# Kernel tuning notes

Measured on AMD Instinct MI355X. Metric: run time of the kernel, lower is better.

Reference implementation:

```python
import jax, jax.numpy as jnp
import numpy as np

B, S, D_IN, D_HID, D_OUT = 32, 512, 768, 3072, 768


def setup_inputs() -> dict:
    key = jax.random.key(0)
    k1, k2, k3, k4 = jax.random.split(key, 4)
    init_k = float(np.sqrt(1.0 / D_IN))
    init_k2 = float(np.sqrt(1.0 / D_HID))
    x = jax.random.normal(k1, (B, S, D_IN), dtype=jnp.float32)
    in_weight = jax.random.uniform(k2, (D_HID, D_IN), dtype=jnp.float32, minval=-init_k, maxval=init_k)
    in_bias = jax.random.uniform(k3, (D_HID,), dtype=jnp.float32, minval=-init_k, maxval=init_k)
    out_weight = jax.random.uniform(k4, (D_HID, D_OUT), dtype=jnp.float32, minval=-init_k2, maxval=init_k2)
    return {"x": x, "in_weight": in_weight, "in_bias": in_bias, "out_weight": out_weight}


def reference(x, in_weight, in_bias, out_weight):
    # flatten leading dims to tokens: [B*S, D_IN]
    lead = x.shape[:-1]
    xt = x.reshape(-1, in_weight.shape[1])
    # hidden = GELU(x @ W_in^T + b)   (in_weight stored [hidden, in])
    h = jax.nn.gelu(jnp.einsum('td,hd->th', xt, in_weight) + in_bias, approximate=False)
    # out = hidden @ W_out            (out_weight stored [hidden, out]; no output bias)
    out = jnp.einsum('th,ho->to', h, out_weight)
    return out.reshape(*lead, out_weight.shape[1])
```

## Files before the change

### kernel.cpp

```cpp
#include <hip/hip_runtime.h>

typedef short bf16x8 __attribute__((ext_vector_type(8)));
typedef float f32x4  __attribute__((ext_vector_type(4)));

__device__ __forceinline__ unsigned short f2bf(float f) {
    unsigned int u = __float_as_uint(f);
    u += 0x7FFFu + ((u >> 16) & 1u);
    return (unsigned short)(u >> 16);
}

__device__ __forceinline__ float gelu_f(float x) {
    float x2 = x * x;
    float u = x * (-1.5957691216f - 0.0713548162f * x2);
    float e = __expf(u);
    return x * __builtin_amdgcn_rcpf(1.0f + e);
}

__global__ void cvt_f32_bf16(const float* __restrict__ in,
                             unsigned short* __restrict__ out, int n4) {
    int stride = gridDim.x * blockDim.x;
    for (int i = blockIdx.x * blockDim.x + threadIdx.x; i < n4; i += stride) {
        float4 v = ((const float4*)in)[i];
        ushort4 r;
        r.x = f2bf(v.x); r.y = f2bf(v.y); r.z = f2bf(v.z); r.w = f2bf(v.w);
        ((ushort4*)out)[i] = r;
    }
}

__global__ void transpose_cvt(const float* __restrict__ in,
                              unsigned short* __restrict__ out, int H, int O) {
    __shared__ float tile[32][33];
    int o0 = blockIdx.x * 32, h0 = blockIdx.y * 32;
    int tx = threadIdx.x, ty = threadIdx.y;
    #pragma unroll
    for (int r = 0; r < 32; r += 8)
        tile[ty + r][tx] = in[(size_t)(h0 + ty + r) * O + o0 + tx];
    __syncthreads();
    #pragma unroll
    for (int r = 0; r < 32; r += 8) {
        int o = ty + r;
        out[(size_t)(o0 + o) * H + h0 + tx] = f2bf(tile[tx][o]);
    }
}

template <int EPI, int K, int N, int BN>
__global__ __launch_bounds__(512, 2) void gemm_bt(
    const unsigned short* __restrict__ A,
    const unsigned short* __restrict__ B,
    const float* __restrict__ bias,
    void* __restrict__ Cp) {
    constexpr int NREP = BN / 64;
    constexpr int BHALF = 32768;
    constexpr int LBUF = BHALF + BN * 128;
    __shared__ __align__(16) char lds[2 * LBUF];
    const int t = threadIdx.x;
    const int w = t >> 6, l = t & 63;
    constexpr int ntiles = N / BN;

    int bid = blockIdx.x;
    int nwg = gridDim.x;
    int wgid = ((nwg & 7) == 0) ? ((bid & 7) * (nwg >> 3) + (bid >> 3)) : bid;
    const int mt = wgid / ntiles, nt = wgid % ntiles;
    const int m0 = mt << 8, n0 = nt * BN;
    const int wr = w >> 2, wc = w & 3;

    const int rA = t >> 3;
    const int sl = (t & 7) ^ (rA & 7);

    auto stage = [&](int kt, char* dst) {
        const int kc = kt * 64 + sl * 8;
        #pragma unroll
        for (int i = 0; i < 4; ++i) {
            const unsigned short* ga = A + (size_t)(m0 + i * 64 + rA) * K + kc;
            char* la = dst + i * 8192 + (w << 10);
            __builtin_amdgcn_global_load_lds((const __attribute__((address_space(1))) void*)ga,
                                             (__attribute__((address_space(3))) void*)la, 16, 0, 0);
        }
        #pragma unroll
        for (int i = 0; i < NREP; ++i) {
            const unsigned short* gb = B + (size_t)(n0 + i * 64 + rA) * K + kc;
            char* lb = dst + BHALF + i * 8192 + (w << 10);
            __builtin_amdgcn_global_load_lds((const __attribute__((address_space(1))) void*)gb,
                                             (__attribute__((address_space(3))) void*)lb, 16, 0, 0);
        }
    };

    const int swz = ((l >> 4) ^ (l & 7)) << 4;
    const int aoff0 = (wr * 128 + (l & 15)) * 128 + swz;
    const int aoffX = aoff0 ^ 64;
    const int boff0 = BHALF + (wc * (BN / 4) + (l & 15)) * 128 + swz;
    const int boffX = boff0 ^ 64;

    f32x4 acc[8][NREP];
    {
        f32x4 z = {0.f, 0.f, 0.f, 0.f};
        #pragma unroll
        for (int i = 0; i < 8; ++i)
            #pragma unroll
            for (int j = 0; j < NREP; ++j) acc[i][j] = z;
    }

    constexpr int NT = K >> 6;
    stage(0, lds);
    __builtin_amdgcn_sched_barrier(0);
    asm volatile("" ::: "memory");
    stage(1, lds + LBUF);

    for (int kt = 0; kt < NT; ++kt) {
        if constexpr (NREP == 4)
            asm volatile("s_waitcnt vmcnt(8)\n\ts_barrier" ::: "memory");
        else
            asm volatile("s_waitcnt vmcnt(7)\n\ts_barrier" ::: "memory");
        __builtin_amdgcn_sched_barrier(0);
        const char* base = lds + (kt & 1) * LBUF;
        bf16x8 av[4][2], bv[NREP][2];
        #pragma unroll
        for (int ni = 0; ni < NREP; ++ni) {
            bv[ni][0] = *(const bf16x8*)(base + boff0 + ni * 2048);
            bv[ni][1] = *(const bf16x8*)(base + boffX + ni * 2048);
        }
        #pragma unroll
        for (int mi = 0; mi < 4; ++mi) {
            av[mi][0] = *(const bf16x8*)(base + aoff0 + mi * 2048);
            av[mi][1] = *(const bf16x8*)(base + aoffX + mi * 2048);
        }
        #pragma unroll
        for (int ks = 0; ks < 2; ++ks)
            #pragma unroll
            for (int mi = 0; mi < 4; ++mi)
                #pragma unroll
                for (int ni = 0; ni < NREP; ++ni)
                    acc[mi][ni] = __builtin_amdgcn_mfma_f32_16x16x32_bf16(
                        av[mi][ks], bv[ni][ks], acc[mi][ni], 0, 0, 0);
        #pragma unroll
        for (int mi = 0; mi < 4; ++mi) {
            av[mi][0] = *(const bf16x8*)(base + aoff0 + (4 + mi) * 2048);
            av[mi][1] = *(const bf16x8*)(base + aoffX + (4 + mi) * 2048);
        }
        #pragma unroll
        for (int ks = 0; ks < 2; ++ks)
            #pragma unroll
            for (int mi = 0; mi < 4; ++mi)
                #pragma unroll
                for (int ni = 0; ni < NREP; ++ni)
                    acc[4 + mi][ni] = __builtin_amdgcn_mfma_f32_16x16x32_bf16(
                        av[mi][ks], bv[ni][ks], acc[4 + mi][ni], 0, 0, 0);
        __builtin_amdgcn_sched_barrier(0);
        asm volatile("s_waitcnt lgkmcnt(0)\n\ts_barrier" ::: "memory");
        __builtin_amdgcn_sched_barrier(0);
        if (kt + 2 < NT) stage(kt + 2, lds + (kt & 1) * LBUF);
    }

    if constexpr (EPI == 0) {
        unsigned short* Cb = (unsigned short*)Cp;
        #pragma unroll
        for (int ni = 0; ni < NREP; ++ni) {
            int col = n0 + wc * (BN / 4) + ni * 16 + (l & 15);
            float bvs = bias[col];
            #pragma unroll
            for (int mi = 0; mi < 8; ++mi) {
                int rbase = m0 + wr * 128 + mi * 16 + ((l >> 4) << 2);
                #pragma unroll
                for (int j = 0; j < 4; ++j) {
                    float v = acc[mi][ni][j] + bvs;
                    Cb[(size_t)(rbase + j) * N + col] = f2bf(gelu_f(v));
                }
            }
        }
    } else {
        float* Cf = (float*)Cp;
        #pragma unroll
        for (int ni = 0; ni < NREP; ++ni) {
            int col = n0 + wc * (BN / 4) + ni * 16 + (l & 15);
            #pragma unroll
            for (int mi = 0; mi < 8; ++mi) {
                int rbase = m0 + wr * 128 + mi * 16 + ((l >> 4) << 2);
                #pragma unroll
                for (int j = 0; j < 4; ++j)
                    Cf[(size_t)(rbase + j) * N + col] = acc[mi][ni][j];
            }
        }
    }
}

extern "C" void kernel_launch(void* const* d_in, const int* in_sizes, int n_in,
                              void* d_out, int out_size, void* d_ws, size_t ws_size,
                              hipStream_t stream) {
    const float* x  = (const float*)d_in[0];
    const float* w1 = (const float*)d_in[1];
    const float* b1 = (const float*)d_in[2];
    const float* w2 = (const float*)d_in[3];
    float* out = (float*)d_out;

    const int T = 16384, DIN = 768, DH = 3072, DOUT = 768;

    unsigned short* xb  = (unsigned short*)d_ws;
    unsigned short* w1b = xb  + (size_t)T * DIN;
    unsigned short* w2t = w1b + (size_t)DH * DIN;
    unsigned short* h   = w2t + (size_t)DOUT * DH;

    size_t fixed = ((size_t)T * DIN + (size_t)DH * DIN + (size_t)DOUT * DH) * 2;
    int CH = T;
    while (CH > 256 && fixed + (size_t)CH * DH * 2 > ws_size) CH >>= 1;

    cvt_f32_bf16<<<2048, 256, 0, stream>>>(x, xb, T * DIN / 4);
    cvt_f32_bf16<<<1024, 256, 0, stream>>>(w1, w1b, DH * DIN / 4);
    transpose_cvt<<<dim3(DOUT / 32, DH / 32), dim3(32, 8), 0, stream>>>(w2, w2t, DH, DOUT);

    for (int c0 = 0; c0 < T; c0 += CH) {
        gemm_bt<0, 768, 3072, 256><<<(CH / 256) * (DH / 256), 512, 0, stream>>>(
            xb + (size_t)c0 * DIN, w1b, b1, h);
        gemm_bt<1, 3072, 768, 192><<<(CH / 256) * (DOUT / 192), 512, 0, stream>>>(
            h, w2t, b1, out + (size_t)c0 * DOUT);
    }
}
```

Measured before the change: 193.7 us.

## Shrink GEMM tiles to 256x128x32 with higher occupancy and a new LDS swizzle

Reworks the bf16 GEMM kernel from 256xBN tiles with K-step 64 to 256x128 tiles with K-step 32. LDS per block drops to 48KB and launch bounds rise to 4 blocks per CU, with an 8-wave 4x2 layout where each wave computes 64x64. The staging and fragment addressing use a new XOR swizzle, and the pipeline always issues a stage so the vmcnt count stays fixed. The aim is more occupancy and better latency hiding, at the cost of less data reuse per tile, more barriers per unit of K, and twice as many blocks.

After: 207.6 us. 1.07x slower.

```diff
diff --git a/kernel.cpp b/kernel.cpp
--- a/kernel.cpp
+++ b/kernel.cpp
@@ -43,143 +43,137 @@
     }
 }
 
-template <int EPI, int K, int N, int BN>
-__global__ __launch_bounds__(512, 2) void gemm_bt(
+template <int EPI, int K, int N>
+__global__ __launch_bounds__(512, 4) void gemm_bt(
     const unsigned short* __restrict__ A,
     const unsigned short* __restrict__ B,
     const float* __restrict__ bias,
     void* __restrict__ Cp) {
-    constexpr int NREP = BN / 64;
-    constexpr int BHALF = 32768;
-    constexpr int LBUF = BHALF + BN * 128;
+    constexpr int BHALF = 16384;
+    constexpr int LBUF  = 24576;
     __shared__ __align__(16) char lds[2 * LBUF];
     const int t = threadIdx.x;
     const int w = t >> 6, l = t & 63;
-    constexpr int ntiles = N / BN;
+    constexpr int ntiles = N >> 7;
 
     int bid = blockIdx.x;
     int nwg = gridDim.x;
     int wgid = ((nwg & 7) == 0) ? ((bid & 7) * (nwg >> 3) + (bid >> 3)) : bid;
     const int mt = wgid / ntiles, nt = wgid % ntiles;
-    const int m0 = mt << 8, n0 = nt * BN;
-    const int wr = w >> 2, wc = w & 3;
-
-    const int rA = t >> 3;
-    const int sl = (t & 7) ^ (rA & 7);
+    const int m0 = mt << 8, n0 = nt << 7;
+    const int wr = w >> 1, wc = w & 1;
 
     auto stage = [&](int kt, char* dst) {
-        const int kc = kt * 64 + sl * 8;
-        #pragma unroll
-        for (int i = 0; i < 4; ++i) {
-            const unsigned short* ga = A + (size_t)(m0 + i * 64 + rA) * K + kc;
-            char* la = dst + i * 8192 + (w << 10);
-            __builtin_amdgcn_global_load_lds((const __attribute__((address_space(1))) void*)ga,
-                                             (__attribute__((address_space(3))) void*)la, 16, 0, 0);
+        const int kb = kt << 5;
+        #pragma unroll
+        for (int p = 0; p < 2; ++p) {
+            int idx = p * 512 + t;
+            int prow = idx >> 3;
+            int lg = (idx & 7) ^ (prow & 7);
+            const unsigned short* ga =
+                A + (size_t)(m0 + (lg >> 2) * 128 + prow) * K + kb + (lg & 3) * 8;
+            __builtin_amdgcn_global_load_lds(
+                (const __attribute__((address_space(1))) void*)ga,
+                (__attribute__((address_space(3))) void*)(dst + idx * 16), 16, 0, 0);
         }
-        #pragma unroll
-        for (int i = 0; i < NREP; ++i) {
-            const unsigned short* gb = B + (size_t)(n0 + i * 64 + rA) * K + kc;
-            char* lb = dst + BHALF + i * 8192 + (w << 10);
-            __builtin_amdgcn_global_load_lds((const __attribute__((address_space(1))) void*)gb,
-                                             (__attribute__((address_space(3))) void*)lb, 16, 0, 0);
+        {
+            int prow = t >> 3;
+            int lg = (t & 7) ^ (prow & 7);
+            const unsigned short* gb =
+                B + (size_t)(n0 + (lg >> 2) * 64 + prow) * K + kb + (lg & 3) * 8;
+            __builtin_amdgcn_global_load_lds(
+                (const __attribute__((address_space(1))) void*)gb,
+                (__attribute__((address_space(3))) void*)(dst + BHALF + t * 16), 16, 0, 0);
         }
     };
 
-    const int swz = ((l >> 4) ^ (l & 7)) << 4;
-    const int aoff0 = (wr * 128 + (l & 15)) * 128 + swz;
-    const int aoffX = aoff0 ^ 64;
-    const int boff0 = BHALF + (wc * (BN / 4) + (l & 15)) * 128 + swz;
-    const int boffX = boff0 ^ 64;
-
-    f32x4 acc[8][NREP];
+    const int ks = l >> 4, lr = l & 15;
+    int aoff[4], boff[4];
+    #pragma unroll
+    for (int mi = 0; mi < 4; ++mi) {
+        int prow = (wr & 1) * 64 + mi * 16 + lr;
+        int lg   = ((wr >> 1) << 2) + ks;
+        aoff[mi] = prow * 128 + ((lg ^ (prow & 7)) << 4);
+    }
+    #pragma unroll
+    for (int ni = 0; ni < 4; ++ni) {
+        int prow = ni * 16 + lr;
+        int lg   = (wc << 2) + ks;
+        boff[ni] = BHALF + prow * 128 + ((lg ^ (prow & 7)) << 4);
+    }
+
+    f32x4 acc[4][4];
     {
         f32x4 z = {0.f, 0.f, 0.f, 0.f};
         #pragma unroll
-        for (int i = 0; i < 8; ++i)
-            #pragma unroll
-            for (int j = 0; j < NREP; ++j) acc[i][j] = z;
-    }
-
-    constexpr int NT = K >> 6;
+        for (int i = 0; i < 4; ++i)
+            #pragma unroll
+            for (int j = 0; j < 4; ++j) acc[i][j] = z;
+    }
+
+    constexpr int NT = K >> 5;
     stage(0, lds);
     __builtin_amdgcn_sched_barrier(0);
     asm volatile("" ::: "memory");
     stage(1, lds + LBUF);
 
     for (int kt = 0; kt < NT; ++kt) {
-        if constexpr (NREP == 4)
-            asm volatile("s_waitcnt vmcnt(8)\n\ts_barrier" ::: "memory");
-        else
-            asm volatile("s_waitcnt vmcnt(7)\n\ts_barrier" ::: "memory");
+        asm volatile("s_waitcnt vmcnt(3)\n\ts_barrier" ::: "memory");
         __builtin_amdgcn_sched_barrier(0);
         const char* base = lds + (kt & 1) * LBUF;
-        bf16x8 av[4][2], bv[NREP][2];
-        #pragma unroll
-        for (int ni = 0; ni < NREP; ++ni) {
-            bv[ni][0] = *(const bf16x8*)(base + boff0 + ni * 2048);
-            bv[ni][1] = *(const bf16x8*)(base + boffX + ni * 2048);
-        }
-        #pragma unroll
-        for (int mi = 0; mi < 4; ++mi) {
-            av[mi][0] = *(const bf16x8*)(base + aoff0 + mi * 2048);
-            av[mi][1] = *(const bf16x8*)(base + aoffX + mi * 2048);
-        }
-        #pragma unroll
-        for (int ks = 0; ks < 2; ++ks)
-            #pragma unroll
-            for (int mi = 0; mi < 4; ++mi)
-                #pragma unroll
-                for (int ni = 0; ni < NREP; ++ni)
-                    acc[mi][ni] = __builtin_amdgcn_mfma_f32_16x16x32_bf16(
-                        av[mi][ks], bv[ni][ks], acc[mi][ni], 0, 0, 0);
-        #pragma unroll
-        for (int mi = 0; mi < 4; ++mi) {
-            av[mi][0] = *(const bf16x8*)(base + aoff0 + (4 + mi) * 2048);
-            av[mi][1] = *(const bf16x8*)(base + aoffX + (4 + mi) * 2048);
-        }
-        #pragma unroll
-        for (int ks = 0; ks < 2; ++ks)
-            #pragma unroll
-            for (int mi = 0; mi < 4; ++mi)
-                #pragma unroll
-                for (int ni = 0; ni < NREP; ++ni)
-                    acc[4 + mi][ni] = __builtin_amdgcn_mfma_f32_16x16x32_bf16(
-                        av[mi][ks], bv[ni][ks], acc[4 + mi][ni], 0, 0, 0);
+        bf16x8 bv[4], av[2];
+        #pragma unroll
+        for (int ni = 0; ni < 4; ++ni) bv[ni] = *(const bf16x8*)(base + boff[ni]);
+        av[0] = *(const bf16x8*)(base + aoff[0]);
+        av[1] = *(const bf16x8*)(base + aoff[1]);
+        #pragma unroll
+        for (int mi = 0; mi < 2; ++mi)
+            #pragma unroll
+            for (int ni = 0; ni < 4; ++ni)
+                acc[mi][ni] = __builtin_amdgcn_mfma_f32_16x16x32_bf16(
+                    av[mi], bv[ni], acc[mi][ni], 0, 0, 0);
+        av[0] = *(const bf16x8*)(base + aoff[2]);
+        av[1] = *(const bf16x8*)(base + aoff[3]);
+        #pragma unroll
+        for (int mi = 0; mi < 2; ++mi)
+            #pragma unroll
+            for (int ni = 0; ni < 4; ++ni)
+                acc[2 + mi][ni] = __builtin_amdgcn_mfma_f32_16x16x32_bf16(
+                    av[mi], bv[ni], acc[2 + mi][ni], 0, 0, 0);
         __builtin_amdgcn_sched_barrier(0);
         asm volatile("s_waitcnt lgkmcnt(0)\n\ts_barrier" ::: "memory");
         __builtin_amdgcn_sched_barrier(0);
-        if (kt + 2 < NT) stage(kt + 2, lds + (kt & 1) * LBUF);
-    }
-
+        stage(kt + 2 < NT ? kt + 2 : NT - 1, lds + (kt & 1) * LBUF);
+    }
+
+    const int colb = n0 + wc * 64 + lr;
     if constexpr (EPI == 0) {
         unsigned short* Cb = (unsigned short*)Cp;
-        #pragma unroll
-        for (int ni = 0; ni < NREP; ++ni) {
-            int col = n0 + wc * (BN / 4) + ni * 16 + (l & 15);
-            float bvs = bias[col];
-            #pragma unroll
-            for (int mi = 0; mi < 8; ++mi) {
-                int rbase = m0 + wr * 128 + mi * 16 + ((l >> 4) << 2);
+        float bvs[4];
+        #pragma unroll
+        for (int ni = 0; ni < 4; ++ni) bvs[ni] = bias[colb + ni * 16];
+        #pragma unroll
+        for (int mi = 0; mi < 4; ++mi)
+            #pragma unroll
+            for (int j = 0; j < 4; ++j) {
+                size_t row = m0 + wr * 64 + mi * 16 + ((l >> 4) << 2) + j;
                 #pragma unroll
-                for (int j = 0; j < 4; ++j) {
-                    float v = acc[mi][ni][j] + bvs;
-                    Cb[(size_t)(rbase + j) * N + col] = f2bf(gelu_f(v));
+                for (int ni = 0; ni < 4; ++ni) {
+                    float v = acc[mi][ni][j] + bvs[ni];
+                    Cb[row * N + colb + ni * 16] = f2bf(gelu_f(v));
                 }
             }
-        }
     } else {
         float* Cf = (float*)Cp;
         #pragma unroll
-        for (int ni = 0; ni < NREP; ++ni) {
-            int col = n0 + wc * (BN / 4) + ni * 16 + (l & 15);
-            #pragma unroll
-            for (int mi = 0; mi < 8; ++mi) {
-                int rbase = m0 + wr * 128 + mi * 16 + ((l >> 4) << 2);
+        for (int mi = 0; mi < 4; ++mi)
+            #pragma unroll
+            for (int j = 0; j < 4; ++j) {
+                size_t row = m0 + wr * 64 + mi * 16 + ((l >> 4) << 2) + j;
                 #pragma unroll
-                for (int j = 0; j < 4; ++j)
-                    Cf[(size_t)(rbase + j) * N + col] = acc[mi][ni][j];
+                for (int ni = 0; ni < 4; ++ni)
+                    Cf[row * N + colb + ni * 16] = acc[mi][ni][j];
             }
-        }
     }
 }
 
@@ -208,9 +202,9 @@
     transpose_cvt<<<dim3(DOUT / 32, DH / 32), dim3(32, 8), 0, stream>>>(w2, w2t, DH, DOUT);
 
     for (int c0 = 0; c0 < T; c0 += CH) {
-        gemm_bt<0, 768, 3072, 256><<<(CH / 256) * (DH / 256), 512, 0, stream>>>(
+        gemm_bt<0, 768, 3072><<<(CH / 256) * (DH / 128), 512, 0, stream>>>(
             xb + (size_t)c0 * DIN, w1b, b1, h);
-        gemm_bt<1, 3072, 768, 192><<<(CH / 256) * (DOUT / 192), 512, 0, stream>>>(
+        gemm_bt<1, 3072, 768><<<(CH / 256) * (DOUT / 128), 512, 0, stream>>>(
             h, w2t, b1, out + (size_t)c0 * DOUT);
     }
 }
```

## Rewrite first GEMM as 4-stage K-half pipeline with interleaved loads and MFMA

Applied to the files above, without the earlier changes.

The first GEMM (x·W_in^T with GELU epilogue) gets a new kernel that splits each 64-wide K tile into two 32-wide halves across four LDS regions. It issues global-to-LDS loads for future halves between MFMA groups, and raises wave priority with s_setprio around the MFMA blocks. The second GEMM now always issues a (clamped, redundant) stage load on the last iterations so the fixed vmcnt wait counts stay valid. The goal is to hide load latency and barrier stalls in the first GEMM, at the cost of 128KB of LDS per block, which may limit occupancy to one block per CU, and some redundant tail loads.

New measurement: 196.4 us. No clear change (+1.4%).

```diff
diff --git a/kernel.cpp b/kernel.cpp
--- a/kernel.cpp
+++ b/kernel.cpp
@@ -43,15 +43,148 @@
     }
 }
 
-template <int EPI, int K, int N, int BN>
-__global__ __launch_bounds__(512, 2) void gemm_bt(
+template <int K, int N>
+__global__ __launch_bounds__(512, 2) void gemm1_8ph(
+    const unsigned short* __restrict__ A,
+    const unsigned short* __restrict__ B,
+    const float* __restrict__ bias,
+    unsigned short* __restrict__ C) {
+    __shared__ __align__(16) char lds[131072];
+    const int t = threadIdx.x;
+    const int w = t >> 6, l = t & 63;
+    constexpr int ntiles = N >> 8;
+
+    int bid = blockIdx.x, nwg = gridDim.x;
+    int wgid = ((nwg & 7) == 0) ? ((bid & 7) * (nwg >> 3) + (bid >> 3)) : bid;
+    const int mt = wgid / ntiles, nt = wgid % ntiles;
+    const int m0 = mt << 8, n0 = nt << 8;
+    const int wr = w >> 2, wc = w & 3;
+
+    const int u1 = t + 512;
+    const int gu0 = (t >> 2) * K + (((t & 3) ^ ((t >> 2) & 3)) << 3);
+    const int gu1 = (u1 >> 2) * K + (((u1 & 3) ^ ((u1 >> 2) & 3)) << 3);
+    const unsigned short* Abase = A + (size_t)m0 * K;
+    const unsigned short* Bbase = B + (size_t)n0 * K;
+
+#define STAGE(PTR, KT, KS, REG) { \
+    const unsigned short* g_ = (PTR) + (KT) * 64 + (KS) * 32; \
+    __builtin_amdgcn_global_load_lds( \
+        (const __attribute__((address_space(1))) void*)(g_ + gu0), \
+        (__attribute__((address_space(3))) void*)(lds + (REG) + t * 16), 16, 0, 0); \
+    __builtin_amdgcn_global_load_lds( \
+        (const __attribute__((address_space(1))) void*)(g_ + gu1), \
+        (__attribute__((address_space(3))) void*)(lds + (REG) + 8192 + t * 16), 16, 0, 0); }
+#define PIN() { __builtin_amdgcn_sched_barrier(0); asm volatile("" ::: "memory"); }
+#define GATE() { asm volatile("s_waitcnt vmcnt(8)\n\ts_barrier" ::: "memory"); \
+                 __builtin_amdgcn_sched_barrier(0); }
+#define LGKM() { __builtin_amdgcn_sched_barrier(0); \
+                 asm volatile("s_waitcnt lgkmcnt(0)" ::: "memory"); \
+                 __builtin_amdgcn_sched_barrier(0); }
+#define RDB(RG) { const char* p_ = lds + (RG) + boffb; \
+    bv[0] = *(const bf16x8*)(p_);        bv[1] = *(const bf16x8*)(p_ + 1024); \
+    bv[2] = *(const bf16x8*)(p_ + 2048); bv[3] = *(const bf16x8*)(p_ + 3072); }
+#define RDA(RG, MH) { const char* p_ = lds + (RG) + aoffb + (MH) * 4096; \
+    av[0] = *(const bf16x8*)(p_);        av[1] = *(const bf16x8*)(p_ + 1024); \
+    av[2] = *(const bf16x8*)(p_ + 2048); av[3] = *(const bf16x8*)(p_ + 3072); }
+#define MFMA16(MB) \
+    _Pragma("unroll") \
+    for (int mi = 0; mi < 4; ++mi) { \
+        _Pragma("unroll") \
+        for (int ni = 0; ni < 4; ++ni) \
+            acc[MB * 4 + mi][ni] = __builtin_amdgcn_mfma_f32_16x16x32_bf16( \
+                av[mi], bv[ni], acc[MB * 4 + mi][ni], 0, 0, 0); \
+    } \
+    __builtin_amdgcn_s_setprio(0); \
+    __builtin_amdgcn_sched_barrier(0);
+
+    const int cR = l >> 4, lr = l & 15;
+    const int swz = (cR ^ (lr & 3)) << 4;
+    const int aoffb = (wr * 128 + lr) * 64 + swz;
+    const int boffb = 32768 + (wc * 64 + lr) * 64 + swz;
+
+    f32x4 acc[8][4];
+    {
+        f32x4 z = {0.f, 0.f, 0.f, 0.f};
+        #pragma unroll
+        for (int i = 0; i < 8; ++i)
+            #pragma unroll
+            for (int j = 0; j < 4; ++j) acc[i][j] = z;
+    }
+    bf16x8 av[4], bv[4];
+
+    constexpr int NTK = K >> 6;
+    constexpr int NT2 = K >> 7;
+
+    STAGE(Abase, 0, 0, 0);             PIN();
+    STAGE(Bbase, 0, 0, 32768);         PIN();
+    STAGE(Abase, 0, 1, 16384);         PIN();
+    STAGE(Bbase, 0, 1, 49152);         PIN();
+    STAGE(Abase, 1, 0, 65536);         PIN();
+    STAGE(Bbase, 1, 0, 98304);         PIN();
+
+    for (int tt = 0; tt < NT2; ++tt) {
+        const int k1 = (2 * tt + 1 < NTK) ? 2 * tt + 1 : NTK - 1;
+        const int k2 = (2 * tt + 2 < NTK) ? 2 * tt + 2 : NTK - 1;
+        const int k3 = (2 * tt + 3 < NTK) ? 2 * tt + 3 : NTK - 1;
+        GATE(); RDB(0); RDA(0, 0);
+        STAGE(Abase, k1, 1, 81920);
+        LGKM(); __builtin_amdgcn_s_setprio(1); MFMA16(0);
+        RDA(0, 1);
+        STAGE(Bbase, k1, 1, 114688);
+        LGKM(); __builtin_amdgcn_s_setprio(1); MFMA16(1);
+        GATE(); RDB(16384); RDA(16384, 0);
+        STAGE(Abase, k2, 0, 0);
+        LGKM(); __builtin_amdgcn_s_setprio(1); MFMA16(0);
+        RDA(16384, 1);
+        STAGE(Bbase, k2, 0, 32768);
+        LGKM(); __builtin_amdgcn_s_setprio(1); MFMA16(1);
+        GATE(); RDB(65536); RDA(65536, 0);
+        STAGE(Abase, k2, 1, 16384);
+        LGKM(); __builtin_amdgcn_s_setprio(1); MFMA16(0);
+        RDA(65536, 1);
+        STAGE(Bbase, k2, 1, 49152);
+        LGKM(); __builtin_amdgcn_s_setprio(1); MFMA16(1);
+        GATE(); RDB(81920); RDA(81920, 0);
+        STAGE(Abase, k3, 0, 65536);
+        LGKM(); __builtin_amdgcn_s_setprio(1); MFMA16(0);
+        RDA(81920, 1);
+        STAGE(Bbase, k3, 0, 98304);
+        LGKM(); __builtin_amdgcn_s_setprio(1); MFMA16(1);
+    }
+#undef STAGE
+#undef PIN
+#undef GATE
+#undef LGKM
+#undef RDB
+#undef RDA
+#undef MFMA16
+
+    const int colb = n0 + wc * 64 + lr;
+    float bvs[4];
+    #pragma unroll
+    for (int ni = 0; ni < 4; ++ni) bvs[ni] = bias[colb + ni * 16];
+    #pragma unroll
+    for (int mi = 0; mi < 8; ++mi)
+        #pragma unroll
+        for (int j = 0; j < 4; ++j) {
+            size_t row = m0 + wr * 128 + mi * 16 + cR * 4 + j;
+            #pragma unroll
+            for (int ni = 0; ni < 4; ++ni) {
+                float v = acc[mi][ni][j] + bvs[ni];
+                C[row * N + colb + ni * 16] = f2bf(gelu_f(v));
+            }
+        }
+}
+
+template <int EPI, int K, int N>
+__global__ __launch_bounds__(512, 2) void gemm_k2(
     const unsigned short* __restrict__ A,
     const unsigned short* __restrict__ B,
     const float* __restrict__ bias,
     void* __restrict__ Cp) {
-    constexpr int NREP = BN / 64;
+    constexpr int BN = 192, NREP = 3;
     constexpr int BHALF = 32768;
-    constexpr int LBUF = BHALF + BN * 128;
+    constexpr int LBUF  = BHALF + BN * 128;
     __shared__ __align__(16) char lds[2 * LBUF];
     const int t = threadIdx.x;
     const int w = t >> 6, l = t & 63;
@@ -107,10 +240,7 @@
     stage(1, lds + LBUF);
 
     for (int kt = 0; kt < NT; ++kt) {
-        if constexpr (NREP == 4)
-            asm volatile("s_waitcnt vmcnt(8)\n\ts_barrier" ::: "memory");
-        else
-            asm volatile("s_waitcnt vmcnt(7)\n\ts_barrier" ::: "memory");
+        asm volatile("s_waitcnt vmcnt(7)\n\ts_barrier" ::: "memory");
         __builtin_amdgcn_sched_barrier(0);
         const char* base = lds + (kt & 1) * LBUF;
         bf16x8 av[4][2], bv[NREP][2];
@@ -125,30 +255,30 @@
             av[mi][1] = *(const bf16x8*)(base + aoffX + mi * 2048);
         }
         #pragma unroll
-        for (int ks = 0; ks < 2; ++ks)
+        for (int ksel = 0; ksel < 2; ++ksel)
             #pragma unroll
             for (int mi = 0; mi < 4; ++mi)
                 #pragma unroll
                 for (int ni = 0; ni < NREP; ++ni)
                     acc[mi][ni] = __builtin_amdgcn_mfma_f32_16x16x32_bf16(
-                        av[mi][ks], bv[ni][ks], acc[mi][ni], 0, 0, 0);
+                        av[mi][ksel], bv[ni][ksel], acc[mi][ni], 0, 0, 0);
         #pragma unroll
         for (int mi = 0; mi < 4; ++mi) {
             av[mi][0] = *(const bf16x8*)(base + aoff0 + (4 + mi) * 2048);
             av[mi][1] = *(const bf16x8*)(base + aoffX + (4 + mi) * 2048);
         }
         #pragma unroll
-        for (int ks = 0; ks < 2; ++ks)
+        for (int ksel = 0; ksel < 2; ++ksel)
             #pragma unroll
             for (int mi = 0; mi < 4; ++mi)
                 #pragma unroll
                 for (int ni = 0; ni < NREP; ++ni)
                     acc[4 + mi][ni] = __builtin_amdgcn_mfma_f32_16x16x32_bf16(
-                        av[mi][ks], bv[ni][ks], acc[4 + mi][ni], 0, 0, 0);
+                        av[mi][ksel], bv[ni][ksel], acc[4 + mi][ni], 0, 0, 0);
         __builtin_amdgcn_sched_barrier(0);
         asm volatile("s_waitcnt lgkmcnt(0)\n\ts_barrier" ::: "memory");
         __builtin_amdgcn_sched_barrier(0);
-        if (kt + 2 < NT) stage(kt + 2, lds + (kt & 1) * LBUF);
+        stage(kt + 2 < NT ? kt + 2 : NT - 1, lds + (kt & 1) * LBUF);
     }
 
     if constexpr (EPI == 0) {
@@ -208,9 +338,9 @@
     transpose_cvt<<<dim3(DOUT / 32, DH / 32), dim3(32, 8), 0, stream>>>(w2, w2t, DH, DOUT);
 
     for (int c0 = 0; c0 < T; c0 += CH) {
-        gemm_bt<0, 768, 3072, 256><<<(CH / 256) * (DH / 256), 512, 0, stream>>>(
+        gemm1_8ph<768, 3072><<<(CH / 256) * (DH / 256), 512, 0, stream>>>(
             xb + (size_t)c0 * DIN, w1b, b1, h);
-        gemm_bt<1, 3072, 768, 192><<<(CH / 256) * (DOUT / 192), 512, 0, stream>>>(
+        gemm_k2<1, 3072, 768><<<(CH / 256) * (DOUT / 192), 512, 0, stream>>>(
             h, w2t, b1, out + (size_t)c0 * DOUT);
     }
 }
```
